# Kernel optimization log

Hardware: AMD Instinct MI355X
Metric: run time of the kernel (lower is better)

Reference implementation:

```python
import jax, jax.numpy as jnp
import numpy as np
import math

INF = 1e12  # constant.INFINITY_NUMBER in the original repo
B, T, D = 64, 512, 1024  # D = 2 * rnn_hidden


def _lin(k, fan_in, fan_out):
    k1, k2 = jax.random.split(k)
    w = jax.random.normal(k1, (fan_in, fan_out), jnp.float32) / np.float32(np.sqrt(fan_in))
    b = jax.random.normal(k2, (fan_out,), jnp.float32) * 0.01
    return w, b


def setup_inputs() -> dict:
    key = jax.random.key(0)
    ks = jax.random.split(key, 12)
    gcn_inputs = jax.random.normal(ks[0], (B, T, D), jnp.float32)
    subj_pos = jax.random.randint(ks[1], (B, T), 0, 8)  # zeros mark the subject span
    obj_pos = jax.random.randint(ks[2], (B, T), 0, 8)
    masks = jax.random.randint(ks[3], (B, T), 0, 2)
    Wq, bq = _lin(ks[4], 2 * D, D)
    Wc, bc = _lin(ks[5], 2 * D, D)
    Wk, bk = _lin(ks[6], D, 1)
    Wm, bm = _lin(ks[7], 3 * D, D)
    WK, bK = _lin(ks[8], D, D)
    WQ, bQ = _lin(ks[9], D, D)
    WV, bV = _lin(ks[10], D, D)
    return dict(gcn_inputs=gcn_inputs, subj_pos=subj_pos, obj_pos=obj_pos, masks=masks,
                Wq=Wq, bq=bq, Wc=Wc, bc=bc, Wk=Wk, bk=bk, Wm=Wm, bm=bm,
                WK=WK, bK=bK, WQ=WQ, bQ=bQ, WV=WV, bV=bV)


def _pool_max(h, mask):
    # mask: True = masked out
    return jnp.max(jnp.where(mask, jnp.float32(-INF), h), axis=1)


def reference(gcn_inputs, subj_pos, obj_pos, masks,
              Wq, bq, Wc, bc, Wk, bk, Wm, bm, WK, bK, WQ, bQ, WV, bV):
    b, t, d = gcn_inputs.shape
    scale = np.float32(1.0 / math.sqrt(d))

    subj_mask = (subj_pos != 0)[:, :, None]  # .eq(0).eq(0)
    subj_out = _pool_max(gcn_inputs, subj_mask)            # [B, D]
    obj_out = _pool_max(gcn_inputs, subj_mask)             # faithful: original also uses subj_mask here
    subj_obj = jnp.concatenate([subj_out, obj_out], axis=1)  # [B, 2D]

    c0 = jnp.zeros((b, d), gcn_inputs.dtype)
    q = jax.nn.relu(subj_obj @ Wq + bq)                    # [B, D]
    tvec = jax.nn.relu(jnp.concatenate([q, c0], axis=1) @ Wc + bc)  # [B, D]
    k = jax.nn.softmax((tvec[:, None, :] * gcn_inputs) @ Wk + bk, axis=1)  # [B, T, 1]
    c = jnp.sum(k * gcn_inputs, axis=1)                    # [B, D]
    m = jax.nn.relu(jnp.concatenate([c, subj_obj], axis=1) @ Wm + bm)[:, None, :]  # [B, 1, D]

    key_h = gcn_inputs @ WK + bK
    query_h = gcn_inputs @ WQ + bQ
    value_h = gcn_inputs @ WV + bV
    scores = jnp.einsum('btd,bsd->bts', key_h, query_h)    # key.bmm(query^T): [B, T, T]

    # att branch: softmax first, THEN scale (faithful to the original quirk)
    att = jax.nn.softmax(scores, axis=2) * scale
    eye = jnp.eye(t, dtype=bool)[None]
    att = jnp.where(eye, jnp.float32(0.0), att).sum(axis=2)  # [B, T]

    # output branch: scale inside softmax
    probs = jax.nn.softmax(scores * scale, axis=2)
    output = m * jnp.einsum('bts,bsd->btd', probs, value_h)  # gated attention output [B, T, D]

    return output, masks[:, :, None], gcn_inputs, att
```

## Files before the change

kernel.cpp:

```cpp
#include <hip/hip_runtime.h>
#include <hip/hip_bf16.h>

#define B_ 64
#define T_ 512
#define D_ 1024
#define NCH 8
#define TCH 64
#define PSTRIDE 12

#define OUT0_OFF 0u
#define OUT1_OFF 33554432u
#define OUT2_OFF 33587200u
#define OUT3_OFF 67141632u

typedef __attribute__((ext_vector_type(8))) short short8;
typedef __attribute__((ext_vector_type(4))) float f32x4;

__device__ __forceinline__ short bf16_of(float x) {
    __hip_bfloat16 h = __float2bfloat16(x);
    return *reinterpret_cast<short*>(&h);
}

__device__ __forceinline__ void gload16(const void* g, void* l) {
    __builtin_amdgcn_global_load_lds(
        (__attribute__((address_space(1))) void*)(g),
        (__attribute__((address_space(3))) void*)(l), 16, 0, 0);
}

__global__ __launch_bounds__(256) void pool_part(const float* __restrict__ gcn,
                                                 const int* __restrict__ subj_pos,
                                                 float* __restrict__ part) {
    __shared__ int keep[TCH];
    int d = blockIdx.x * 256 + threadIdx.x;
    int ch = blockIdx.y, b = blockIdx.z;
    if (threadIdx.x < TCH) keep[threadIdx.x] = (subj_pos[b * T_ + ch * TCH + threadIdx.x] == 0);
    __syncthreads();
    const float* gb = gcn + ((size_t)b * T_ + ch * TCH) * D_ + d;
    float mx = -1e12f;
    #pragma unroll 4
    for (int i = 0; i < TCH; i++) {
        float v = gb[(size_t)i * D_];
        if (keep[i]) mx = fmaxf(mx, v);
    }
    part[((size_t)b * PSTRIDE + ch) * D_ + d] = mx;
}

__global__ __launch_bounds__(256) void pool_red(const float* __restrict__ part,
                                                float* __restrict__ subj) {
    int d = blockIdx.x * 256 + threadIdx.x;
    int b = blockIdx.y;
    float mx = -1e12f;
    #pragma unroll
    for (int ch = 0; ch < NCH; ch++) mx = fmaxf(mx, part[((size_t)b * PSTRIDE + ch) * D_ + d]);
    subj[(size_t)b * D_ + d] = mx;
}

__global__ __launch_bounds__(256) void mv_part(const float* __restrict__ x0,
                                               const float* __restrict__ x1,
                                               const float* __restrict__ W,
                                               float* __restrict__ part) {
    __shared__ float xs[256];
    int j = blockIdx.x * 256 + threadIdx.x;
    int ch = blockIdx.y, b = blockIdx.z;
    int gi = ch * 256 + threadIdx.x;
    xs[threadIdx.x] = (gi < D_) ? x0[(size_t)b * D_ + gi]
                                : x1[(size_t)b * D_ + ((gi - D_) & (D_ - 1))];
    __syncthreads();
    const float* Wp = W + (size_t)ch * 256 * D_ + j;
    float a0 = 0.f, a1 = 0.f, a2 = 0.f, a3 = 0.f;
    #pragma unroll 4
    for (int i = 0; i < 256; i += 4) {
        a0 += xs[i] * Wp[(size_t)i * D_];
        a1 += xs[i + 1] * Wp[(size_t)(i + 1) * D_];
        a2 += xs[i + 2] * Wp[(size_t)(i + 2) * D_];
        a3 += xs[i + 3] * Wp[(size_t)(i + 3) * D_];
    }
    part[((size_t)b * PSTRIDE + ch) * D_ + j] = (a0 + a1) + (a2 + a3);
}

__global__ __launch_bounds__(256) void mv_red(const float* __restrict__ part,
                                              const float* __restrict__ bias,
                                              float* __restrict__ y, int nch) {
    int j = blockIdx.x * 256 + threadIdx.x;
    int b = blockIdx.y;
    float acc = bias[j];
    for (int ch = 0; ch < nch; ch++) acc += part[((size_t)b * PSTRIDE + ch) * D_ + j];
    y[(size_t)b * D_ + j] = fmaxf(acc, 0.f);
}

__global__ __launch_bounds__(256) void vecs_kernel(const float* __restrict__ WKm,
                                                   const float* __restrict__ WQm,
                                                   const float* __restrict__ bKv,
                                                   const float* __restrict__ bQv,
                                                   float* __restrict__ u,
                                                   float* __restrict__ w,
                                                   float* __restrict__ alpha) {
    int tid = threadIdx.x, wave = tid >> 6, lane = tid & 63;
    int row = blockIdx.x * 4 + wave;
    float s1 = 0.f, s2 = 0.f;
    for (int c = lane; c < D_; c += 64) {
        s1 += WKm[(size_t)row * D_ + c] * bQv[c];
        s2 += WQm[(size_t)row * D_ + c] * bKv[c];
    }
    #pragma unroll
    for (int off = 32; off; off >>= 1) {
        s1 += __shfl_xor(s1, off);
        s2 += __shfl_xor(s2, off);
    }
    if (lane == 0) { u[row] = s1; w[row] = s2; }
    if (blockIdx.x == 0 && wave == 0) {
        float a = 0.f;
        for (int c = lane; c < D_; c += 64) a += bKv[c] * bQv[c];
        #pragma unroll
        for (int off = 32; off; off >>= 1) a += __shfl_xor(a, off);
        if (lane == 0) alpha[0] = a;
    }
}

__global__ __launch_bounds__(256) void att_dots(const float* __restrict__ gcn,
                                                const float* __restrict__ u,
                                                const float* __restrict__ w,
                                                const float* __restrict__ tv,
                                                const float* __restrict__ Wk,
                                                const float* __restrict__ alpha,
                                                const float* __restrict__ bk,
                                                float* __restrict__ Gu,
                                                float* __restrict__ Gw,
                                                float* __restrict__ lg) {
    __shared__ float su[D_], sw[D_], s2[D_];
    int tid = threadIdx.x, wave = tid >> 6, lane = tid & 63;
    size_t row0 = (size_t)blockIdx.x * 4;
    int b = (int)(row0 >> 9);
    for (int c = tid; c < D_; c += 256) {
        su[c] = u[c];
        sw[c] = w[c];
        s2[c] = tv[(size_t)b * D_ + c] * Wk[c];
    }
    __syncthreads();
    size_t row = row0 + wave;
    const float* g = gcn + row * D_;
    float d1 = 0.f, d2 = 0.f, d3 = 0.f;
    for (int c = lane; c < D_; c += 64) {
        float gv = g[c];
        d1 += gv * su[c];
        d2 += gv * sw[c];
        d3 += gv * s2[c];
    }
    #pragma unroll
    for (int off = 32; off; off >>= 1) {
        d1 += __shfl_xor(d1, off);
        d2 += __shfl_xor(d2, off);
        d3 += __shfl_xor(d3, off);
    }
    if (lane == 0) {
        Gu[row] = d1 + alpha[0];
        Gw[row] = d2;
        lg[row] = d3 + bk[0];
    }
}

__global__ __launch_bounds__(256) void ksoftmax_kernel(float* __restrict__ lg) {
    __shared__ float red[4];
    int b = blockIdx.x, tid = threadIdx.x;
    int wave = tid >> 6, lane = tid & 63;
    float* L = lg + (size_t)b * T_;
    float v0 = L[tid], v1 = L[tid + 256];
    float mx = fmaxf(v0, v1);
    #pragma unroll
    for (int off = 32; off; off >>= 1) mx = fmaxf(mx, __shfl_xor(mx, off));
    if (lane == 0) red[wave] = mx;
    __syncthreads();
    mx = fmaxf(fmaxf(red[0], red[1]), fmaxf(red[2], red[3]));
    __syncthreads();
    float e0 = expf(v0 - mx), e1 = expf(v1 - mx);
    float zs = e0 + e1;
    #pragma unroll
    for (int off = 32; off; off >>= 1) zs += __shfl_xor(zs, off);
    if (lane == 0) red[wave] = zs;
    __syncthreads();
    float invZ = 1.f / (red[0] + red[1] + red[2] + red[3]);
    L[tid] = e0 * invZ;
    L[tid + 256] = e1 * invZ;
}

__global__ __launch_bounds__(256) void csum_part(const float* __restrict__ gcn,
                                                 const float* __restrict__ k,
                                                 float* __restrict__ part) {
    __shared__ float kv[TCH];
    int d = blockIdx.x * 256 + threadIdx.x;
    int ch = blockIdx.y, b = blockIdx.z;
    if (threadIdx.x < TCH) kv[threadIdx.x] = k[(size_t)b * T_ + ch * TCH + threadIdx.x];
    __syncthreads();
    const float* gb = gcn + ((size_t)b * T_ + ch * TCH) * D_ + d;
    float acc = 0.f;
    #pragma unroll 4
    for (int i = 0; i < TCH; i++) acc += kv[i] * gb[(size_t)i * D_];
    part[((size_t)b * PSTRIDE + ch) * D_ + d] = acc;
}

__global__ __launch_bounds__(256) void csum_reduce(const float* __restrict__ part,
                                                   float* __restrict__ cbuf) {
    int d = blockIdx.x * 256 + threadIdx.x;
    int b = blockIdx.y;
    float acc = 0.f;
    #pragma unroll
    for (int ch = 0; ch < NCH; ch++) acc += part[((size_t)b * PSTRIDE + ch) * D_ + d];
    cbuf[(size_t)b * D_ + d] = acc;
}

__global__ __launch_bounds__(256) void cast_kernel(const float* __restrict__ in,
                                                   short* __restrict__ out, size_t n8) {
    size_t i = (size_t)blockIdx.x * 256 + threadIdx.x;
    size_t stride = (size_t)gridDim.x * 256;
    for (; i < n8; i += stride) {
        f32x4 v0 = ((const f32x4*)in)[2 * i];
        f32x4 v1 = ((const f32x4*)in)[2 * i + 1];
        short8 o;
        #pragma unroll
        for (int j = 0; j < 4; j++) {
            o[j] = bf16_of(v0[j]);
            o[4 + j] = bf16_of(v1[j]);
        }
        ((short8*)out)[i] = o;
    }
}

__global__ __launch_bounds__(256) void prep_kernel(const float* __restrict__ in,
                                                   short* __restrict__ gs,
                                                   short* __restrict__ gt,
                                                   float* __restrict__ o2) {
    __shared__ float tile[32][33];
    int z = blockIdx.z;
    in += (size_t)z * T_ * D_;
    gs += (size_t)z * T_ * D_;
    gt += (size_t)z * D_ * T_;
    o2 += (size_t)z * T_ * D_;
    int c0 = blockIdx.x * 32, r0 = blockIdx.y * 32;
    int tx = threadIdx.x & 31, ty = threadIdx.x >> 5;
    #pragma unroll
    for (int i = 0; i < 4; i++) {
        int r = ty + i * 8;
        size_t idx = (size_t)(r0 + r) * D_ + c0 + tx;
        float v = in[idx];
        tile[r][tx] = v;
        o2[idx] = v;
        gs[idx] = bf16_of(v);
    }
    __syncthreads();
    #pragma unroll
    for (int i = 0; i < 4; i++) {
        int c = ty + i * 8;
        gt[(size_t)(c0 + c) * T_ + r0 + tx] = bf16_of(tile[tx][c]);
    }
}

__global__ __launch_bounds__(256) void transpose_kernel(const float* __restrict__ in, size_t sIn,
                                                        short* __restrict__ out, size_t sOut,
                                                        int R, int C) {
    __shared__ float tile[32][33];
    int z = blockIdx.z;
    in += (size_t)z * sIn;
    out += (size_t)z * sOut;
    int c0 = blockIdx.x * 32, r0 = blockIdx.y * 32;
    int tx = threadIdx.x & 31, ty = threadIdx.x >> 5;
    #pragma unroll
    for (int i = 0; i < 4; i++) {
        int r = ty + i * 8;
        tile[r][tx] = in[(size_t)(r0 + r) * C + c0 + tx];
    }
    __syncthreads();
    #pragma unroll
    for (int i = 0; i < 4; i++) {
        int c = ty + i * 8;
        out[(size_t)(c0 + c) * R + r0 + tx] = bf16_of(tile[tx][c]);
    }
}

template <int MODE>
__global__ __launch_bounds__(256) void gemm_nt(
        const short* __restrict__ A, size_t sAz,
        const short* __restrict__ Bt, size_t sBz,
        int K, int ldout,
        float* __restrict__ Cf, short* __restrict__ Cb, size_t sCz,
        const float* __restrict__ e1, const float* __restrict__ e2) {
    __shared__ __align__(16) short As[128 * 64];
    __shared__ __align__(16) short Bs[128 * 64];
    int z = blockIdx.z;
    A += (size_t)z * sAz;
    Bt += (size_t)z * sBz;
    int t = threadIdx.x;
    int lane = t & 63, wave = t >> 6;
    int wr = wave >> 1, wc = wave & 1;
    size_t rowBase = (size_t)blockIdx.x * 128;
    size_t colBase = (size_t)blockIdx.y * 128;

    int rlo = lane >> 3;
    int src16 = (lane & 7) ^ rlo;
    const short* gA[4];
    const short* gB[4];
    short* lA[4];
    short* lB[4];
    #pragma unroll
    for (int i = 0; i < 4; i++) {
        int ch = wave * 4 + i;
        int row = ch * 8 + rlo;
        gA[i] = A + (rowBase + row) * (size_t)K + src16 * 8;
        gB[i] = Bt + (colBase + row) * (size_t)K + src16 * 8;
        lA[i] = As + ch * 512;
        lB[i] = Bs + ch * 512;
    }

    f32x4 acc[4][4] = {};
    for (int kb = 0; kb < K; kb += 64) {
        __syncthreads();
        #pragma unroll
        for (int i = 0; i < 4; i++) {
            gload16(gA[i] + kb, lA[i]);
            gload16(gB[i] + kb, lB[i]);
        }
        __syncthreads();
        #pragma unroll
        for (int kk = 0; kk < 2; kk++) {
            int ko16 = kk * 4 + (lane >> 4);
            int sw = ko16 ^ (lane & 7);
            short8 af[4], bfr[4];
            #pragma unroll
            for (int i = 0; i < 4; i++) {
                int row = wr * 64 + i * 16 + (lane & 15);
                af[i] = *(const short8*)(As + row * 64 + (sw << 3));
            }
            #pragma unroll
            for (int j = 0; j < 4; j++) {
                int row = wc * 64 + j * 16 + (lane & 15);
                bfr[j] = *(const short8*)(Bs + row * 64 + (sw << 3));
            }
            #pragma unroll
            for (int i = 0; i < 4; i++)
                #pragma unroll
                for (int j = 0; j < 4; j++)
                    acc[i][j] = __builtin_amdgcn_mfma_f32_16x16x32_bf16(af[i], bfr[j], acc[i][j], 0, 0, 0);
        }
    }
    #pragma unroll
    for (int i = 0; i < 4; i++) {
        #pragma unroll
        for (int j = 0; j < 4; j++) {
            #pragma unroll
            for (int r = 0; r < 4; r++) {
                size_t row = rowBase + wr * 64 + i * 16 + (lane >> 4) * 4 + r;
                size_t col = colBase + wc * 64 + j * 16 + (lane & 15);
                float v = acc[i][j][r];
                if (MODE == 0) {
                    Cf[z * sCz + row * ldout + col] = v;
                } else if (MODE == 1) {
                    Cf[z * sCz + row * ldout + col] = v + e1[z * T_ + row] + e2[z * T_ + col];
                } else if (MODE == 2) {
                    Cb[z * sCz + row * ldout + col] = bf16_of(v);
                } else {
                    Cf[z * sCz + row * ldout + col] = (v + e1[col]) * e2[(size_t)z * D_ + col];
                }
            }
        }
    }
}

__global__ __launch_bounds__(64) void softmax_att(const float* __restrict__ S,
                                                  short* __restrict__ probs,
                                                  float* __restrict__ att) {
    const float SCALE = 0.03125f;
    int t = blockIdx.x, z = blockIdx.y, lane = threadIdx.x;
    const float* row = S + ((size_t)z * T_ + t) * T_;
    short* prow = probs + ((size_t)z * T_ + t) * T_;
    float v[8];
    float mx = -1e30f;
    #pragma unroll
    for (int k = 0; k < 8; k++) {
        v[k] = row[lane + k * 64];
        mx = fmaxf(mx, v[k]);
    }
    #pragma unroll
    for (int off = 32; off; off >>= 1) mx = fmaxf(mx, __shfl_xor(mx, off));
    float z1 = 0.f, z2 = 0.f, dg = 0.f;
    #pragma unroll
    for (int k = 0; k < 8; k++) {
        float x = v[k] - mx;
        float e1 = expf(x);
        float e2 = expf(x * SCALE);
        z1 += e1;
        z2 += e2;
        if (lane + k * 64 == t) dg = e1;
        v[k] = e2;
    }
    #pragma unroll
    for (int off = 32; off; off >>= 1) {
        z1 += __shfl_xor(z1, off);
        z2 += __shfl_xor(z2, off);
        dg += __shfl_xor(dg, off);
    }
    float inv2 = 1.f / z2;
    #pragma unroll
    for (int k = 0; k < 8; k++) prow[lane + k * 64] = bf16_of(v[k] * inv2);
    if (lane == 0) att[z * T_ + t] = SCALE * (1.f - dg / z1);
}

__global__ __launch_bounds__(256) void masks_kernel(const int* __restrict__ masks,
                                                    float* __restrict__ out_masks) {
    int i = blockIdx.x * 256 + threadIdx.x;
    if (i < B_ * T_) out_masks[i] = (float)masks[i];
}

extern "C" void kernel_launch(void* const* d_in, const int* in_sizes, int n_in,
                              void* d_out, int out_size, void* d_ws, size_t ws_size,
                              hipStream_t stream) {
    const float* gcn = (const float*)d_in[0];
    const int* subj_pos = (const int*)d_in[1];
    const int* masks = (const int*)d_in[3];
    const float* Wq = (const float*)d_in[4];
    const float* bq = (const float*)d_in[5];
    const float* Wc = (const float*)d_in[6];
    const float* bc = (const float*)d_in[7];
    const float* Wk = (const float*)d_in[8];
    const float* bk = (const float*)d_in[9];
    const float* Wm = (const float*)d_in[10];
    const float* bm = (const float*)d_in[11];
    const float* WK = (const float*)d_in[12];
    const float* bK = (const float*)d_in[13];
    const float* WQ = (const float*)d_in[14];
    const float* bQ = (const float*)d_in[15];
    const float* WV = (const float*)d_in[16];
    const float* bV = (const float*)d_in[17];

    float* out = (float*)d_out;

    char* p = (char*)d_ws;
    auto alloc = [&](size_t bytes) {
        char* r = p;
        p += (bytes + 255) & ~(size_t)255;
        return r;
    };
    float* subj = (float*)alloc(B_ * D_ * 4);
    float* qv   = (float*)alloc(B_ * D_ * 4);
    float* tv   = (float*)alloc(B_ * D_ * 4);
    float* cb   = (float*)alloc(B_ * D_ * 4);
    float* mb   = (float*)alloc(B_ * D_ * 4);
    float* u    = (float*)alloc(D_ * 4);
    float* w    = (float*)alloc(D_ * 4);
    float* alph = (float*)alloc(256);
    float* Gu   = (float*)alloc(B_ * T_ * 4);
    float* Gw   = (float*)alloc(B_ * T_ * 4);
    float* lg   = (float*)alloc(B_ * T_ * 4);
    float* part = (float*)alloc((size_t)B_ * PSTRIDE * D_ * 4);
    float* Pt   = (float*)alloc((size_t)D_ * D_ * 4);
    short* WKb  = (short*)alloc((size_t)D_ * D_ * 2);
    short* WQb  = (short*)alloc((size_t)D_ * D_ * 2);
    short* Ptb  = (short*)alloc((size_t)D_ * D_ * 2);
    short* WVt  = (short*)alloc((size_t)D_ * D_ * 2);

    size_t fixedBytes = (size_t)(p - (char*)d_ws);
    const size_t perBatch = (size_t)T_ * D_ * 2
                          + (size_t)T_ * D_ * 2
                          + (size_t)D_ * T_ * 2
                          + (size_t)T_ * T_ * 4
                          + (size_t)T_ * T_ * 2
                          + (size_t)T_ * D_ * 2;
    int nc = 64;
    while (nc > 1 && fixedBytes + (size_t)nc * perBatch + 4096 > ws_size) nc >>= 1;

    short* Gs_c    = (short*)alloc((size_t)nc * T_ * D_ * 2);
    short* Ys_c    = (short*)alloc((size_t)nc * T_ * D_ * 2);
    short* Gt_c    = (short*)alloc((size_t)nc * D_ * T_ * 2);
    float* S_c     = (float*)alloc((size_t)nc * T_ * T_ * 4);
    short* probs_c = (short*)alloc((size_t)nc * T_ * T_ * 2);
    short* Zs_c    = (short*)alloc((size_t)nc * T_ * D_ * 2);

    pool_part<<<dim3(D_ / 256, NCH, B_), 256, 0, stream>>>(gcn, subj_pos, part);
    pool_red<<<dim3(D_ / 256, B_), 256, 0, stream>>>(part, subj);
    mv_part<<<dim3(D_ / 256, 8, B_), 256, 0, stream>>>(subj, subj, Wq, part);
    mv_red<<<dim3(D_ / 256, B_), 256, 0, stream>>>(part, bq, qv, 8);
    mv_part<<<dim3(D_ / 256, 4, B_), 256, 0, stream>>>(qv, qv, Wc, part);
    mv_red<<<dim3(D_ / 256, B_), 256, 0, stream>>>(part, bc, tv, 4);
    vecs_kernel<<<D_ / 4, 256, 0, stream>>>(WK, WQ, bK, bQ, u, w, alph);
    att_dots<<<B_ * T_ / 4, 256, 0, stream>>>(gcn, u, w, tv, Wk, alph, bk, Gu, Gw, lg);
    ksoftmax_kernel<<<B_, 256, 0, stream>>>(lg);
    csum_part<<<dim3(D_ / 256, NCH, B_), 256, 0, stream>>>(gcn, lg, part);
    csum_reduce<<<dim3(D_ / 256, B_), 256, 0, stream>>>(part, cb);
    mv_part<<<dim3(D_ / 256, 12, B_), 256, 0, stream>>>(cb, subj, Wm, part);
    mv_red<<<dim3(D_ / 256, B_), 256, 0, stream>>>(part, bm, mb, 12);

    cast_kernel<<<512, 256, 0, stream>>>(WK, WKb, (size_t)D_ * D_ / 8);
    cast_kernel<<<512, 256, 0, stream>>>(WQ, WQb, (size_t)D_ * D_ / 8);
    gemm_nt<0><<<dim3(8, 8, 1), 256, 0, stream>>>(WQb, 0, WKb, 0, D_, D_,
                                                  Pt, nullptr, 0, nullptr, nullptr);
    cast_kernel<<<512, 256, 0, stream>>>(Pt, Ptb, (size_t)D_ * D_ / 8);
    transpose_kernel<<<dim3(32, 32, 1), 256, 0, stream>>>(WV, 0, WVt, 0, D_, D_);

    for (int b0 = 0; b0 < B_; b0 += nc) {
        const float* Gc = gcn + (size_t)b0 * T_ * D_;
        prep_kernel<<<dim3(D_ / 32, T_ / 32, nc), 256, 0, stream>>>(
            Gc, Gs_c, Gt_c, out + OUT2_OFF + (size_t)b0 * T_ * D_);
        gemm_nt<2><<<dim3(nc * T_ / 128, D_ / 128, 1), 256, 0, stream>>>(
            Gs_c, 0, Ptb, 0, D_, D_, nullptr, Ys_c, 0, nullptr, nullptr);
        gemm_nt<1><<<dim3(T_ / 128, T_ / 128, nc), 256, 0, stream>>>(
            Ys_c, (size_t)T_ * D_, Gs_c, (size_t)T_ * D_, D_, T_,
            S_c, nullptr, (size_t)T_ * T_, Gu + (size_t)b0 * T_, Gw + (size_t)b0 * T_);
        softmax_att<<<dim3(T_, nc), 64, 0, stream>>>(S_c, probs_c, out + OUT3_OFF + (size_t)b0 * T_);
        gemm_nt<2><<<dim3(T_ / 128, D_ / 128, nc), 256, 0, stream>>>(
            probs_c, (size_t)T_ * T_, Gt_c, (size_t)D_ * T_, T_, D_,
            nullptr, Zs_c, (size_t)T_ * D_, nullptr, nullptr);
        gemm_nt<3><<<dim3(T_ / 128, D_ / 128, nc), 256, 0, stream>>>(
            Zs_c, (size_t)T_ * D_, WVt, 0, D_, D_,
            out + OUT0_OFF + (size_t)b0 * T_ * D_, nullptr, (size_t)T_ * D_,
            bV, mb + (size_t)b0 * D_);
    }

    masks_kernel<<<(B_ * T_ + 255) / 256, 256, 0, stream>>>(masks, out + OUT1_OFF);
}
```

Before: 656.0 us.

## Vectorize small kernels, swizzle GEMM block order, pack softmax rows per block

Converts the pooling, matrix-vector, column-sum, dot-product and prep kernels to float4 loads and stores, with each thread handling four columns so one block covers the whole hidden dimension. Adds a block-index swizzle in the GEMM so neighbouring blocks are spread across the grid, aimed at better cache locality across XCDs. Packs four softmax rows into each 256-thread block instead of one row per 64-thread block. The goal is fewer memory instructions and better load efficiency, at the cost of fewer blocks in the small kernels, which lowers their parallelism.

Result: faster. 631.3 us (-3.8%).

```diff
diff --git a/kernel.cpp b/kernel.cpp
--- a/kernel.cpp
+++ b/kernel.cpp
@@ -14,6 +14,7 @@
 #define OUT3_OFF 67141632u
 
 typedef __attribute__((ext_vector_type(8))) short short8;
+typedef __attribute__((ext_vector_type(4))) short short4v;
 typedef __attribute__((ext_vector_type(4))) float f32x4;
 
 __device__ __forceinline__ short bf16_of(float x) {
@@ -31,28 +32,39 @@
                                                  const int* __restrict__ subj_pos,
                                                  float* __restrict__ part) {
     __shared__ int keep[TCH];
-    int d = blockIdx.x * 256 + threadIdx.x;
+    int d = threadIdx.x * 4;
     int ch = blockIdx.y, b = blockIdx.z;
     if (threadIdx.x < TCH) keep[threadIdx.x] = (subj_pos[b * T_ + ch * TCH + threadIdx.x] == 0);
     __syncthreads();
     const float* gb = gcn + ((size_t)b * T_ + ch * TCH) * D_ + d;
-    float mx = -1e12f;
+    f32x4 mx = {-1e12f, -1e12f, -1e12f, -1e12f};
     #pragma unroll 4
     for (int i = 0; i < TCH; i++) {
-        float v = gb[(size_t)i * D_];
-        if (keep[i]) mx = fmaxf(mx, v);
-    }
-    part[((size_t)b * PSTRIDE + ch) * D_ + d] = mx;
+        f32x4 v = *(const f32x4*)(gb + (size_t)i * D_);
+        if (keep[i]) {
+            mx[0] = fmaxf(mx[0], v[0]);
+            mx[1] = fmaxf(mx[1], v[1]);
+            mx[2] = fmaxf(mx[2], v[2]);
+            mx[3] = fmaxf(mx[3], v[3]);
+        }
+    }
+    *(f32x4*)(part + ((size_t)b * PSTRIDE + ch) * D_ + d) = mx;
 }
 
 __global__ __launch_bounds__(256) void pool_red(const float* __restrict__ part,
                                                 float* __restrict__ subj) {
-    int d = blockIdx.x * 256 + threadIdx.x;
+    int d = threadIdx.x * 4;
     int b = blockIdx.y;
-    float mx = -1e12f;
-    #pragma unroll
-    for (int ch = 0; ch < NCH; ch++) mx = fmaxf(mx, part[((size_t)b * PSTRIDE + ch) * D_ + d]);
-    subj[(size_t)b * D_ + d] = mx;
+    f32x4 mx = {-1e12f, -1e12f, -1e12f, -1e12f};
+    #pragma unroll
+    for (int ch = 0; ch < NCH; ch++) {
+        f32x4 v = *(const f32x4*)(part + ((size_t)b * PSTRIDE + ch) * D_ + d);
+        mx[0] = fmaxf(mx[0], v[0]);
+        mx[1] = fmaxf(mx[1], v[1]);
+        mx[2] = fmaxf(mx[2], v[2]);
+        mx[3] = fmaxf(mx[3], v[3]);
+    }
+    *(f32x4*)(subj + (size_t)b * D_ + d) = mx;
 }
 
 __global__ __launch_bounds__(256) void mv_part(const float* __restrict__ x0,
@@ -60,32 +72,35 @@
                                                const float* __restrict__ W,
                                                float* __restrict__ part) {
     __shared__ float xs[256];
-    int j = blockIdx.x * 256 + threadIdx.x;
+    int j = threadIdx.x * 4;
     int ch = blockIdx.y, b = blockIdx.z;
     int gi = ch * 256 + threadIdx.x;
     xs[threadIdx.x] = (gi < D_) ? x0[(size_t)b * D_ + gi]
                                 : x1[(size_t)b * D_ + ((gi - D_) & (D_ - 1))];
     __syncthreads();
     const float* Wp = W + (size_t)ch * 256 * D_ + j;
-    float a0 = 0.f, a1 = 0.f, a2 = 0.f, a3 = 0.f;
+    f32x4 a0 = {}, a1 = {};
     #pragma unroll 4
-    for (int i = 0; i < 256; i += 4) {
-        a0 += xs[i] * Wp[(size_t)i * D_];
-        a1 += xs[i + 1] * Wp[(size_t)(i + 1) * D_];
-        a2 += xs[i + 2] * Wp[(size_t)(i + 2) * D_];
-        a3 += xs[i + 3] * Wp[(size_t)(i + 3) * D_];
-    }
-    part[((size_t)b * PSTRIDE + ch) * D_ + j] = (a0 + a1) + (a2 + a3);
+    for (int i = 0; i < 256; i += 2) {
+        f32x4 w0 = *(const f32x4*)(Wp + (size_t)i * D_);
+        f32x4 w1 = *(const f32x4*)(Wp + (size_t)(i + 1) * D_);
+        a0 += xs[i] * w0;
+        a1 += xs[i + 1] * w1;
+    }
+    *(f32x4*)(part + ((size_t)b * PSTRIDE + ch) * D_ + j) = a0 + a1;
 }
 
 __global__ __launch_bounds__(256) void mv_red(const float* __restrict__ part,
                                               const float* __restrict__ bias,
                                               float* __restrict__ y, int nch) {
-    int j = blockIdx.x * 256 + threadIdx.x;
+    int j = threadIdx.x * 4;
     int b = blockIdx.y;
-    float acc = bias[j];
-    for (int ch = 0; ch < nch; ch++) acc += part[((size_t)b * PSTRIDE + ch) * D_ + j];
-    y[(size_t)b * D_ + j] = fmaxf(acc, 0.f);
+    f32x4 acc = *(const f32x4*)(bias + j);
+    for (int ch = 0; ch < nch; ch++)
+        acc += *(const f32x4*)(part + ((size_t)b * PSTRIDE + ch) * D_ + j);
+    #pragma unroll
+    for (int q = 0; q < 4; q++) acc[q] = fmaxf(acc[q], 0.f);
+    *(f32x4*)(y + (size_t)b * D_ + j) = acc;
 }
 
 __global__ __launch_bounds__(256) void vecs_kernel(const float* __restrict__ WKm,
@@ -140,11 +155,19 @@
     size_t row = row0 + wave;
     const float* g = gcn + row * D_;
     float d1 = 0.f, d2 = 0.f, d3 = 0.f;
-    for (int c = lane; c < D_; c += 64) {
-        float gv = g[c];
-        d1 += gv * su[c];
-        d2 += gv * sw[c];
-        d3 += gv * s2[c];
+    #pragma unroll
+    for (int it = 0; it < 4; it++) {
+        int c = lane * 4 + it * 256;
+        f32x4 gv = *(const f32x4*)(g + c);
+        f32x4 uu = *(const f32x4*)(su + c);
+        f32x4 ww = *(const f32x4*)(sw + c);
+        f32x4 kk = *(const f32x4*)(s2 + c);
+        #pragma unroll
+        for (int q = 0; q < 4; q++) {
+            d1 += gv[q] * uu[q];
+            d2 += gv[q] * ww[q];
+            d3 += gv[q] * kk[q];
+        }
     }
     #pragma unroll
     for (int off = 32; off; off >>= 1) {
@@ -187,25 +210,26 @@
                                                  const float* __restrict__ k,
                                                  float* __restrict__ part) {
     __shared__ float kv[TCH];
-    int d = blockIdx.x * 256 + threadIdx.x;
+    int d = threadIdx.x * 4;
     int ch = blockIdx.y, b = blockIdx.z;
     if (threadIdx.x < TCH) kv[threadIdx.x] = k[(size_t)b * T_ + ch * TCH + threadIdx.x];
     __syncthreads();
     const float* gb = gcn + ((size_t)b * T_ + ch * TCH) * D_ + d;
-    float acc = 0.f;
+    f32x4 acc = {};
     #pragma unroll 4
-    for (int i = 0; i < TCH; i++) acc += kv[i] * gb[(size_t)i * D_];
-    part[((size_t)b * PSTRIDE + ch) * D_ + d] = acc;
+    for (int i = 0; i < TCH; i++) acc += kv[i] * *(const f32x4*)(gb + (size_t)i * D_);
+    *(f32x4*)(part + ((size_t)b * PSTRIDE + ch) * D_ + d) = acc;
 }
 
 __global__ __launch_bounds__(256) void csum_reduce(const float* __restrict__ part,
                                                    float* __restrict__ cbuf) {
-    int d = blockIdx.x * 256 + threadIdx.x;
+    int d = threadIdx.x * 4;
     int b = blockIdx.y;
-    float acc = 0.f;
-    #pragma unroll
-    for (int ch = 0; ch < NCH; ch++) acc += part[((size_t)b * PSTRIDE + ch) * D_ + d];
-    cbuf[(size_t)b * D_ + d] = acc;
+    f32x4 acc = {};
+    #pragma unroll
+    for (int ch = 0; ch < NCH; ch++)
+        acc += *(const f32x4*)(part + ((size_t)b * PSTRIDE + ch) * D_ + d);
+    *(f32x4*)(cbuf + (size_t)b * D_ + d) = acc;
 }
 
 __global__ __launch_bounds__(256) void cast_kernel(const float* __restrict__ in,
@@ -236,21 +260,25 @@
     gt += (size_t)z * D_ * T_;
     o2 += (size_t)z * T_ * D_;
     int c0 = blockIdx.x * 32, r0 = blockIdx.y * 32;
-    int tx = threadIdx.x & 31, ty = threadIdx.x >> 5;
+    int tx = threadIdx.x & 7, ty = threadIdx.x >> 3;
+    {
+        size_t idx = (size_t)(r0 + ty) * D_ + c0 + tx * 4;
+        f32x4 v = *(const f32x4*)(in + idx);
+        *(f32x4*)(o2 + idx) = v;
+        short4v s;
+        #pragma unroll
+        for (int q = 0; q < 4; q++) {
+            s[q] = bf16_of(v[q]);
+            tile[ty][tx * 4 + q] = v[q];
+        }
+        *(short4v*)(gs + idx) = s;
+    }
+    __syncthreads();
+    int tx2 = threadIdx.x & 31, ty2 = threadIdx.x >> 5;
     #pragma unroll
     for (int i = 0; i < 4; i++) {
-        int r = ty + i * 8;
-        size_t idx = (size_t)(r0 + r) * D_ + c0 + tx;
-        float v = in[idx];
-        tile[r][tx] = v;
-        o2[idx] = v;
-        gs[idx] = bf16_of(v);
-    }
-    __syncthreads();
-    #pragma unroll
-    for (int i = 0; i < 4; i++) {
-        int c = ty + i * 8;
-        gt[(size_t)(c0 + c) * T_ + r0 + tx] = bf16_of(tile[tx][c]);
+        int c = ty2 + i * 8;
+        gt[(size_t)(c0 + c) * T_ + r0 + tx2] = bf16_of(tile[tx2][c]);
     }
 }
 
@@ -285,14 +313,23 @@
         const float* __restrict__ e1, const float* __restrict__ e2) {
     __shared__ __align__(16) short As[128 * 64];
     __shared__ __align__(16) short Bs[128 * 64];
-    int z = blockIdx.z;
+    unsigned gx = gridDim.x, gy = gridDim.y;
+    unsigned lin = blockIdx.x + gx * (blockIdx.y + gy * blockIdx.z);
+    unsigned tot = gx * gy * gridDim.z;
+    unsigned swz = (lin & 7u) * (tot >> 3) + (lin >> 3);
+    unsigned bx = swz % gx;
+    unsigned tmp = swz / gx;
+    unsigned by = tmp % gy;
+    unsigned bz = tmp / gy;
+
+    int z = bz;
     A += (size_t)z * sAz;
     Bt += (size_t)z * sBz;
     int t = threadIdx.x;
     int lane = t & 63, wave = t >> 6;
     int wr = wave >> 1, wc = wave & 1;
-    size_t rowBase = (size_t)blockIdx.x * 128;
-    size_t colBase = (size_t)blockIdx.y * 128;
+    size_t rowBase = (size_t)bx * 128;
+    size_t colBase = (size_t)by * 128;
 
     int rlo = lane >> 3;
     int src16 = (lane & 7) ^ rlo;
@@ -364,11 +401,12 @@
     }
 }
 
-__global__ __launch_bounds__(64) void softmax_att(const float* __restrict__ S,
-                                                  short* __restrict__ probs,
-                                                  float* __restrict__ att) {
+__global__ __launch_bounds__(256) void softmax_att(const float* __restrict__ S,
+                                                   short* __restrict__ probs,
+                                                   float* __restrict__ att) {
     const float SCALE = 0.03125f;
-    int t = blockIdx.x, z = blockIdx.y, lane = threadIdx.x;
+    int wave = threadIdx.x >> 6, lane = threadIdx.x & 63;
+    int t = blockIdx.x * 4 + wave, z = blockIdx.y;
     const float* row = S + ((size_t)z * T_ + t) * T_;
     short* prow = probs + ((size_t)z * T_ + t) * T_;
     float v[8];
@@ -473,19 +511,19 @@
     short* probs_c = (short*)alloc((size_t)nc * T_ * T_ * 2);
     short* Zs_c    = (short*)alloc((size_t)nc * T_ * D_ * 2);
 
-    pool_part<<<dim3(D_ / 256, NCH, B_), 256, 0, stream>>>(gcn, subj_pos, part);
-    pool_red<<<dim3(D_ / 256, B_), 256, 0, stream>>>(part, subj);
-    mv_part<<<dim3(D_ / 256, 8, B_), 256, 0, stream>>>(subj, subj, Wq, part);
-    mv_red<<<dim3(D_ / 256, B_), 256, 0, stream>>>(part, bq, qv, 8);
-    mv_part<<<dim3(D_ / 256, 4, B_), 256, 0, stream>>>(qv, qv, Wc, part);
-    mv_red<<<dim3(D_ / 256, B_), 256, 0, stream>>>(part, bc, tv, 4);
+    pool_part<<<dim3(1, NCH, B_), 256, 0, stream>>>(gcn, subj_pos, part);
+    pool_red<<<dim3(1, B_), 256, 0, stream>>>(part, subj);
+    mv_part<<<dim3(1, 8, B_), 256, 0, stream>>>(subj, subj, Wq, part);
+    mv_red<<<dim3(1, B_), 256, 0, stream>>>(part, bq, qv, 8);
+    mv_part<<<dim3(1, 4, B_), 256, 0, stream>>>(qv, qv, Wc, part);
+    mv_red<<<dim3(1, B_), 256, 0, stream>>>(part, bc, tv, 4);
     vecs_kernel<<<D_ / 4, 256, 0, stream>>>(WK, WQ, bK, bQ, u, w, alph);
     att_dots<<<B_ * T_ / 4, 256, 0, stream>>>(gcn, u, w, tv, Wk, alph, bk, Gu, Gw, lg);
     ksoftmax_kernel<<<B_, 256, 0, stream>>>(lg);
-    csum_part<<<dim3(D_ / 256, NCH, B_), 256, 0, stream>>>(gcn, lg, part);
-    csum_reduce<<<dim3(D_ / 256, B_), 256, 0, stream>>>(part, cb);
-    mv_part<<<dim3(D_ / 256, 12, B_), 256, 0, stream>>>(cb, subj, Wm, part);
-    mv_red<<<dim3(D_ / 256, B_), 256, 0, stream>>>(part, bm, mb, 12);
+    csum_part<<<dim3(1, NCH, B_), 256, 0, stream>>>(gcn, lg, part);
+    csum_reduce<<<dim3(1, B_), 256, 0, stream>>>(part, cb);
+    mv_part<<<dim3(1, 12, B_), 256, 0, stream>>>(cb, subj, Wm, part);
+    mv_red<<<dim3(1, B_), 256, 0, stream>>>(part, bm, mb, 12);
 
     cast_kernel<<<512, 256, 0, stream>>>(WK, WKb, (size_t)D_ * D_ / 8);
     cast_kernel<<<512, 256, 0, stream>>>(WQ, WQb, (size_t)D_ * D_ / 8);
@@ -503,7 +541,7 @@
         gemm_nt<1><<<dim3(T_ / 128, T_ / 128, nc), 256, 0, stream>>>(
             Ys_c, (size_t)T_ * D_, Gs_c, (size_t)T_ * D_, D_, T_,
             S_c, nullptr, (size_t)T_ * T_, Gu + (size_t)b0 * T_, Gw + (size_t)b0 * T_);
-        softmax_att<<<dim3(T_, nc), 64, 0, stream>>>(S_c, probs_c, out + OUT3_OFF + (size_t)b0 * T_);
+        softmax_att<<<dim3(T_ / 4, nc), 256, 0, stream>>>(S_c, probs_c, out + OUT3_OFF + (size_t)b0 * T_);
         gemm_nt<2><<<dim3(T_ / 128, D_ / 128, nc), 256, 0, stream>>>(
             probs_c, (size_t)T_ * T_, Gt_c, (size_t)D_ * T_, T_, D_,
             nullptr, Zs_c, (size_t)T_ * D_, nullptr, nullptr);
```
